# Kernel tuning notes

Measured on AMD Instinct MI355X. Metric: run time of the kernel, lower is better.

Reference implementation:

```python
import jax, jax.numpy as jnp
import numpy as np
import itertools

D_MODEL = 1024
TEMP = 0.3


def _hypercube(n):
    # all 2^n corners of {-1,+1}^n, matching generate_hypercube(n)
    return jnp.asarray(np.array(list(itertools.product([-1.0, 1.0], repeat=n)), dtype=np.float32))


def setup_inputs() -> dict:
    key = jax.random.key(0)
    ks = jax.random.split(key, 12)
    B, T, D = 8, 4096, D_MODEL
    s = 0.02
    return {
        "x": jax.random.normal(ks[0], (B, T, D), dtype=jnp.float32),
        "codes_l1": _hypercube(3),   # (8, 3)
        "codes_l2": _hypercube(6),   # (64, 6)
        "w_to_l1": jax.random.normal(ks[1], (D, 3), dtype=jnp.float32) * s,
        "w_from_l1": jax.random.normal(ks[2], (3, D), dtype=jnp.float32) * s,
        "w_to_l2": jax.random.normal(ks[3], (D, 6), dtype=jnp.float32) * s,
        "w_from_l2": jax.random.normal(ks[4], (6, D), dtype=jnp.float32) * s,
        "w_to_l3u": jax.random.normal(ks[5], (D, 6), dtype=jnp.float32) * s,
        "w_to_l3l": jax.random.normal(ks[6], (D, 6), dtype=jnp.float32) * s,
        "w_from_l3": jax.random.normal(ks[7], (12, D), dtype=jnp.float32) * s,
        "w_gate": jax.random.normal(ks[8], (D, 3), dtype=jnp.float32) * s,
        "b_gate": jnp.zeros((3,), dtype=jnp.float32),
        "temp_l1": jnp.log(jnp.float32(TEMP)),
        "temp_l2": jnp.log(jnp.float32(TEMP * 0.7)),
        "temp_l3": jnp.log(jnp.float32(TEMP * 0.5)),
        "scale_l1": jnp.float32(0.1),
        "scale_l2": jnp.float32(0.05),
        "scale_l3": jnp.float32(0.02),
    }


def _soft_quantize(z, codes, temp_log):
    # z: (B, T, n); codes: (K, n) -> (B, T, n)
    temp = jnp.clip(jnp.exp(temp_log), 0.01, 5.0)
    # Euclidean cdist: (B, T, K)
    dists = jnp.sqrt(jnp.sum(jnp.square(z[..., None, :] - codes), axis=-1))
    weights = jax.nn.softmax(-dists / temp, axis=-1)
    return weights @ codes


def reference(x, codes_l1, codes_l2, w_to_l1, w_from_l1, w_to_l2, w_from_l2,
              w_to_l3u, w_to_l3l, w_from_l3, w_gate, b_gate,
              temp_l1, temp_l2, temp_l3, scale_l1, scale_l2, scale_l3):
    # gate uses detached x
    gate = jax.nn.softmax(jax.lax.stop_gradient(x) @ w_gate + b_gate, axis=-1)  # (B,T,3)

    # Level 1: Z2^3
    q1 = _soft_quantize(x @ w_to_l1, codes_l1, temp_l1)
    out_l1 = q1 @ w_from_l1

    # Level 2: Z2^6
    q2 = _soft_quantize(x @ w_to_l2, codes_l2, temp_l2)
    out_l2 = q2 @ w_from_l2

    # Level 3: Z2^12 = two Z2^6 halves
    q3u = _soft_quantize(x @ w_to_l3u, codes_l2, temp_l3)
    q3l = _soft_quantize(x @ w_to_l3l, codes_l2, temp_l3)
    out_l3 = jnp.concatenate([q3u, q3l], axis=-1) @ w_from_l3

    out = (gate[..., 0:1] * scale_l1 * out_l1
           + gate[..., 1:2] * scale_l2 * out_l2
           + gate[..., 2:3] * scale_l3 * out_l3)
    gate_means = jnp.mean(gate, axis=(0, 1))  # stats dict analogue: (3,)
    return x + out, gate_means
```

## Files before the change

### kernel.cpp

```cpp
#include <hip/hip_runtime.h>
#include <stdint.h>


#define DM 1024
#define TPB 64
#define OUT_OFF ((size_t)33554432)
#define NTOK 32768
#define NSLOT 32
#define WSA_OFF 32768

typedef float f32x4 __attribute__((ext_vector_type(4)));
typedef short bf16x8 __attribute__((ext_vector_type(8)));

typedef const __attribute__((address_space(1))) unsigned int* gas1_t;
typedef __attribute__((address_space(3))) unsigned int* las3_t;

__device__ __forceinline__ void gl_lds16(const void* g, void* l){
  __builtin_amdgcn_global_load_lds((gas1_t)g, (las3_t)l, 16, 0, 0);
}

__device__ __forceinline__ short f2bf(float f){
  unsigned u = __builtin_bit_cast(unsigned, f);
  unsigned r = u + 0x7fffu + ((u >> 16) & 1u);
  return (short)(r >> 16);
}

template<int NB>
__device__ __forceinline__ void softq(const float* z, float invt, float* q){
  constexpr int K = 1 << NB;
  float d[K];
  float dmin = 3.4e38f;
#pragma unroll
  for (int j = 0; j < K; ++j){
    float acc = 0.f;
#pragma unroll
    for (int i = 0; i < NB; ++i){
      float c = ((j >> (NB-1-i)) & 1) ? 1.f : -1.f;
      float t = z[i] - c;
      acc = fmaf(t, t, acc);
    }
    float dj = sqrtf(acc);
    d[j] = dj;
    dmin = fminf(dmin, dj);
  }
  float S = 0.f;
  float s1[NB];
#pragma unroll
  for (int i = 0; i < NB; ++i) s1[i] = 0.f;
#pragma unroll
  for (int j = 0; j < K; ++j){
    float wj = __expf((dmin - d[j]) * invt);
    S += wj;
#pragma unroll
    for (int i = 0; i < NB; ++i)
      if ((j >> (NB-1-i)) & 1) s1[i] += wj;
  }
  float rS = 1.f / S;
#pragma unroll
  for (int i = 0; i < NB; ++i) q[i] = 2.f * s1[i] * rS - 1.f;
}

__global__ __launch_bounds__(256) void pack_kernel(
    const float* __restrict__ w_to_l1,  const float* __restrict__ w_to_l2,
    const float* __restrict__ w_to_l3u, const float* __restrict__ w_to_l3l,
    const float* __restrict__ w_gate,
    const float* __restrict__ w_from_l1, const float* __restrict__ w_from_l2,
    const float* __restrict__ w_from_l3,
    short* __restrict__ wsF, float* __restrict__ wsA)
{
  int base = blockIdx.x*4096 + threadIdx.x*16;
#pragma unroll
  for (int q = 0; q < 16; ++q){
    int e = base + q;
    float v;
    if (e < 32768){
      int s  = e >> 10;
      int nf = (e >> 9) & 1;
      int ll = (e >> 3) & 63;
      int j  = e & 7;
      int k  = s*32 + ((ll >> 4) << 3) + j;
      int n  = nf*16 + (ll & 15);
      if      (n < 3)  v = w_gate  [k*3 + n];
      else if (n < 6)  v = w_to_l1 [k*3 + (n-3)];
      else if (n < 12) v = w_to_l2 [k*6 + (n-6)];
      else if (n < 18) v = w_to_l3u[k*6 + (n-12)];
      else if (n < 24) v = w_to_l3l[k*6 + (n-18)];
      else             v = 0.f;
    } else {
      int e2  = e - 32768;
      int f   = e2 / 384;
      int rem = e2 - f*384;
      int ll  = rem >> 3;
      int j   = e2 & 7;
      int k   = ((ll >> 4) << 3) + j;
      int dd  = f*16 + (ll & 15);
      if      (k < 3)  v = w_from_l1[k*DM + dd];
      else if (k < 9)  v = w_from_l2[(k-3)*DM + dd];
      else if (k < 21) v = w_from_l3[(k-9)*DM + dd];
      else             v = 0.f;
    }
    wsF[e] = f2bf(v);
  }
  if (blockIdx.x == 0){
    wsA[threadIdx.x]       = 0.f;
    wsA[threadIdx.x + 256] = 0.f;
  }
}

__global__ __launch_bounds__(256, 2) void hq8_kernel(
    const float* __restrict__ x, const short* __restrict__ wsF,
    const float* __restrict__ b_gate,
    const float* __restrict__ t1p, const float* __restrict__ t2p, const float* __restrict__ t3p,
    const float* __restrict__ s1p, const float* __restrict__ s2p, const float* __restrict__ s3p,
    float* __restrict__ wsA, float* __restrict__ out)
{
  __shared__ alignas(16) char smem[65536];

  const int tid  = threadIdx.x;
  const int l    = tid & 63;
  const int wv   = tid >> 6;
  const int kg   = l >> 4;
  const int ln16 = l & 15;
  const int tokBase = blockIdx.x * TPB + wv*16;

  char*  W  = smem + wv*16384;
  float* Cw = reinterpret_cast<float*>(W + 8192);
  float* Pw = reinterpret_cast<float*>(W + 12544);
  short* Vw = reinterpret_cast<short*>(W + 14720);

  const float invt1 = 1.f / fminf(fmaxf(__expf(t1p[0]), 0.01f), 5.0f);
  const float invt2 = 1.f / fminf(fmaxf(__expf(t2p[0]), 0.01f), 5.0f);
  const float invt3 = 1.f / fminf(fmaxf(__expf(t3p[0]), 0.01f), 5.0f);
  const float s1v = s1p[0], s2v = s2p[0], s3v = s3p[0];
  const float bg0 = b_gate[0], bg1 = b_gate[1], bg2 = b_gate[2];

  {
    f32x4 acc0 = {0.f,0.f,0.f,0.f}, acc1 = {0.f,0.f,0.f,0.f};
    const int lr0 = l >> 5;
    const int cbp = l & 31;
#pragma unroll
    for (int i = 0; i < 8; ++i){
      int lr = i*2 + lr0;
      gl_lds16(x + (size_t)(tokBase + lr)*DM + (cbp ^ (lr & 7))*4,
               W + i*1024 + l*16);
    }
#pragma unroll
    for (int t = 0; t < 8; ++t){
      const int buf = t & 1;
      bf16x8 bfr[8];
#pragma unroll
      for (int s2 = 0; s2 < 8; ++s2)
        bfr[s2] = *reinterpret_cast<const bf16x8*>(&wsF[(t*8 + s2)*512 + l*8]);
      __builtin_amdgcn_sched_barrier(0);
      if (t < 7){
#pragma unroll
        for (int i = 0; i < 8; ++i){
          int lr = i*2 + lr0;
          gl_lds16(x + (size_t)(tokBase + lr)*DM + (t+1)*128 + (cbp ^ (lr & 7))*4,
                   W + (buf^1)*8192 + i*1024 + l*16);
        }
        asm volatile("s_waitcnt vmcnt(8)" ::: "memory");
      } else {
        asm volatile("s_waitcnt vmcnt(0)" ::: "memory");
      }
      const char* abase = W + buf*8192 + ln16*512;
#pragma unroll
      for (int s = 0; s < 4; ++s){
        float4 xa = *reinterpret_cast<const float4*>(abase + ((s*8 + kg*2 + 0) ^ (ln16 & 7))*16);
        float4 xb = *reinterpret_cast<const float4*>(abase + ((s*8 + kg*2 + 1) ^ (ln16 & 7))*16);
        bf16x8 af;
        af[0]=f2bf(xa.x); af[1]=f2bf(xa.y); af[2]=f2bf(xa.z); af[3]=f2bf(xa.w);
        af[4]=f2bf(xb.x); af[5]=f2bf(xb.y); af[6]=f2bf(xb.z); af[7]=f2bf(xb.w);
        acc0 = __builtin_amdgcn_mfma_f32_16x16x32_bf16(af, bfr[s*2+0], acc0, 0, 0, 0);
        acc1 = __builtin_amdgcn_mfma_f32_16x16x32_bf16(af, bfr[s*2+1], acc1, 0, 0, 0);
      }
    }
#pragma unroll
    for (int r = 0; r < 4; ++r){
      int row = kg*4 + r;
      Pw[row*34 + ln16]      = acc0[r];
      Pw[row*34 + 16 + ln16] = acc1[r];
    }
  }

  const short* wsFC = wsF + 32768;
  bf16x8 bwc0={0,0,0,0,0,0,0,0}, bwc1=bwc0, bwc2=bwc0, bwc3=bwc0;
  {
#pragma unroll
    for (int j = 0; j < 4; ++j){
      int lr = j*4 + (l >> 4);
      gl_lds16(x + (size_t)(tokBase + lr)*DM + ((l & 15) ^ (lr & 7))*4,
               W + j*1024 + l*16);
    }
    if (kg < 3){
      bwc0 = *reinterpret_cast<const bf16x8*>(&wsFC[0*384 + l*8]);
      bwc1 = *reinterpret_cast<const bf16x8*>(&wsFC[1*384 + l*8]);
      bwc2 = *reinterpret_cast<const bf16x8*>(&wsFC[2*384 + l*8]);
      bwc3 = *reinterpret_cast<const bf16x8*>(&wsFC[3*384 + l*8]);
    }
#pragma unroll
    for (int j = 0; j < 4; ++j){
      int lr = j*4 + (l >> 4);
      gl_lds16(x + (size_t)(tokBase + lr)*DM + 64 + ((l & 15) ^ (lr & 7))*4,
               W + 4096 + j*1024 + l*16);
    }
  }

  float qv[6] = {0,0,0,0,0,0};
  float myscale = 0.f, g1s2v = 0.f, g2s3v = 0.f;
  float sg0 = 0.f, sg1 = 0.f, sg2 = 0.f;
  {
    const int t  = ln16;
    const int gi = kg;
    const int base = (gi == 3) ? 0 : 6 + gi*6;
    float z[6];
#pragma unroll
    for (int i = 0; i < 6; ++i) z[i] = Pw[t*34 + base + i];
    if (gi == 3){
      float g0l = z[0] + bg0;
      float g1l = z[1] + bg1;
      float g2l = z[2] + bg2;
      float m  = fmaxf(g0l, fmaxf(g1l, g2l));
      float e0 = __expf(g0l - m), e1 = __expf(g1l - m), e2 = __expf(g2l - m);
      float rs = 1.f / (e0 + e1 + e2);
      float g0 = e0*rs, g1 = e1*rs, g2 = e2*rs;
      myscale = g0 * s1v;
      g1s2v   = g1 * s2v;
      g2s3v   = g2 * s3v;
      float z1[3] = {z[3], z[4], z[5]};
      softq<3>(z1, invt1, qv);
      sg0 = g0; sg1 = g1; sg2 = g2;
#pragma unroll
      for (int mm = 1; mm < 16; mm <<= 1){
        sg0 += __shfl_xor(sg0, mm, 64);
        sg1 += __shfl_xor(sg1, mm, 64);
        sg2 += __shfl_xor(sg2, mm, 64);
      }
    } else {
      float invt = (gi == 0) ? invt2 : invt3;
      softq<6>(z, invt, qv);
    }
    float gs1 = __shfl(g1s2v, 48 + t, 64);
    float gs2 = __shfl(g2s3v, 48 + t, 64);
    if (gi == 3){
#pragma unroll
      for (int i = 0; i < 3; ++i) Vw[t*40 + i] = f2bf(myscale * qv[i]);
      Vw[t*40 + 21] = 0; Vw[t*40 + 22] = 0; Vw[t*40 + 23] = 0;
    } else {
      float sc = (gi == 0) ? gs1 : gs2;
      int voff = 3 + gi*6;
#pragma unroll
      for (int i = 0; i < 6; ++i) Vw[t*40 + voff + i] = f2bf(sc * qv[i]);
    }
  }

  bf16x8 aV = {0,0,0,0,0,0,0,0};
  if (kg < 3)
    aV = *reinterpret_cast<const bf16x8*>(&Vw[ln16*40 + kg*8]);
  const f32x4 z4 = {0.f,0.f,0.f,0.f};
  const int rl = l >> 2;
  const int cs = l & 3;

#pragma unroll
  for (int c = 0; c < 16; ++c){
    if (c == 0 || c == 15) asm volatile("s_waitcnt vmcnt(4)" ::: "memory");
    else                   asm volatile("s_waitcnt vmcnt(8)" ::: "memory");
    __builtin_amdgcn_sched_barrier(0);
    {
      f32x4 d0 = __builtin_amdgcn_mfma_f32_16x16x32_bf16(aV, bwc0, z4, 0, 0, 0);
      f32x4 d1 = __builtin_amdgcn_mfma_f32_16x16x32_bf16(aV, bwc1, z4, 0, 0, 0);
      f32x4 d2 = __builtin_amdgcn_mfma_f32_16x16x32_bf16(aV, bwc2, z4, 0, 0, 0);
      f32x4 d3 = __builtin_amdgcn_mfma_f32_16x16x32_bf16(aV, bwc3, z4, 0, 0, 0);
#pragma unroll
      for (int r = 0; r < 4; ++r){
        int rowb = (kg*4 + r)*68;
        Cw[rowb +  0 + ln16] = d0[r];
        Cw[rowb + 16 + ln16] = d1[r];
        Cw[rowb + 32 + ln16] = d2[r];
        Cw[rowb + 48 + ln16] = d3[r];
      }
    }
    __builtin_amdgcn_sched_barrier(0);
    bf16x8 bwn0 = bwc0, bwn1 = bwc1, bwn2 = bwc2, bwn3 = bwc3;
    if (c < 15 && kg < 3){
      bwn0 = *reinterpret_cast<const bf16x8*>(&wsFC[((c+1)*4+0)*384 + l*8]);
      bwn1 = *reinterpret_cast<const bf16x8*>(&wsFC[((c+1)*4+1)*384 + l*8]);
      bwn2 = *reinterpret_cast<const bf16x8*>(&wsFC[((c+1)*4+2)*384 + l*8]);
      bwn3 = *reinterpret_cast<const bf16x8*>(&wsFC[((c+1)*4+3)*384 + l*8]);
    }
    __builtin_amdgcn_sched_barrier(0);
    asm volatile("s_waitcnt lgkmcnt(0)" ::: "memory");
    __builtin_amdgcn_sched_barrier(0);
#pragma unroll
    for (int q = 0; q < 4; ++q){
      int bi = cs + 4*q;
      f32x4 xv = *reinterpret_cast<const f32x4*>(
          W + (c & 1)*4096 + rl*256 + ((bi ^ (rl & 7)))*16);
      f32x4 cv = *reinterpret_cast<const f32x4*>(&Cw[rl*68 + bi*4]);
      f32x4 ov = xv + cv;
      *reinterpret_cast<f32x4*>(&out[(size_t)(tokBase + rl)*DM + c*64 + bi*4]) = ov;
    }
    __builtin_amdgcn_sched_barrier(0);
    if (c < 14){
#pragma unroll
      for (int j = 0; j < 4; ++j){
        int lr = j*4 + (l >> 4);
        gl_lds16(x + (size_t)(tokBase + lr)*DM + (c+2)*64 + ((l & 15) ^ (lr & 7))*4,
                 W + (c & 1)*4096 + j*1024 + l*16);
      }
    }
    bwc0 = bwn0; bwc1 = bwn1; bwc2 = bwn2; bwc3 = bwn3;
  }

  if (l == 48){
    float* slot = wsA + ((blockIdx.x*4 + wv) & (NSLOT-1))*16;
    atomicAdd(slot + 0, sg0);
    atomicAdd(slot + 1, sg1);
    atomicAdd(slot + 2, sg2);
  }
}

__global__ void finalize_kernel(const float* __restrict__ wsA, float* __restrict__ out){
  if (threadIdx.x < 3){
    float s = 0.f;
    for (int j = 0; j < NSLOT; ++j) s += wsA[j*16 + threadIdx.x];
    out[OUT_OFF + threadIdx.x] = s * (1.f / (float)NTOK);
  }
}

extern "C" void kernel_launch(void* const* d_in, const int* in_sizes, int n_in,
                              void* d_out, int out_size, void* d_ws, size_t ws_size,
                              hipStream_t stream){
  (void)in_sizes; (void)n_in; (void)ws_size; (void)out_size;
  const float* x         = (const float*)d_in[0];
  const float* w_to_l1   = (const float*)d_in[3];
  const float* w_from_l1 = (const float*)d_in[4];
  const float* w_to_l2   = (const float*)d_in[5];
  const float* w_from_l2 = (const float*)d_in[6];
  const float* w_to_l3u  = (const float*)d_in[7];
  const float* w_to_l3l  = (const float*)d_in[8];
  const float* w_from_l3 = (const float*)d_in[9];
  const float* w_gate    = (const float*)d_in[10];
  const float* b_gate    = (const float*)d_in[11];
  const float* t1 = (const float*)d_in[12];
  const float* t2 = (const float*)d_in[13];
  const float* t3 = (const float*)d_in[14];
  const float* s1 = (const float*)d_in[15];
  const float* s2 = (const float*)d_in[16];
  const float* s3 = (const float*)d_in[17];
  float* out  = (float*)d_out;
  short* wsF  = (short*)d_ws;
  float* wsA  = (float*)d_ws + WSA_OFF;

  pack_kernel<<<dim3(14), dim3(256), 0, stream>>>(
      w_to_l1, w_to_l2, w_to_l3u, w_to_l3l, w_gate,
      w_from_l1, w_from_l2, w_from_l3, wsF, wsA);
  hq8_kernel<<<dim3(512), dim3(256), 0, stream>>>(
      x, wsF, b_gate, t1, t2, t3, s1, s2, s3, wsA, out);
  finalize_kernel<<<dim3(1), dim3(64), 0, stream>>>(wsA, out);
}
```

Measured before the change: 81.03 us.

## Split fused kernel into down-projection and up-projection kernels via workspace

Splits the single fused kernel into two. The first kernel computes the projections, gate and soft-quantization and writes the per-token scaled code vectors to a workspace. The second kernel reads those vectors back, does the up-projection MFMA and adds x to produce the output. This simplifies each kernel's pipeline and register use, but it reads x a second time from memory (128MB extra traffic) and drops the hand-tuned double-buffered residual prefetch.

```diff
diff --git a/kernel.cpp b/kernel.cpp
--- a/kernel.cpp
+++ b/kernel.cpp
@@ -3,11 +3,11 @@
 
 
 #define DM 1024
-#define TPB 64
 #define OUT_OFF ((size_t)33554432)
 #define NTOK 32768
 #define NSLOT 32
-#define WSA_OFF 32768
+#define WSV_OFF 65536
+#define WSA_OFFF 557056
 
 typedef float f32x4 __attribute__((ext_vector_type(4)));
 typedef short bf16x8 __attribute__((ext_vector_type(8)));
@@ -107,12 +107,63 @@
   }
 }
 
-__global__ __launch_bounds__(256, 2) void hq8_kernel(
+__device__ __forceinline__ void quant16(const float* Pw, short* Vw, int l,
+    float invt1, float invt2, float invt3, float s1v, float s2v, float s3v,
+    float bg0, float bg1, float bg2, float& sg0, float& sg1, float& sg2)
+{
+  const int t  = l & 15;
+  const int gi = l >> 4;
+  const int base = (gi == 3) ? 0 : 6 + gi*6;
+  float z[6];
+#pragma unroll
+  for (int i = 0; i < 6; ++i) z[i] = Pw[t*34 + base + i];
+  float qv[6] = {0,0,0,0,0,0};
+  float myscale = 0.f, g1s2v = 0.f, g2s3v = 0.f;
+  if (gi == 3){
+    float g0l = z[0] + bg0;
+    float g1l = z[1] + bg1;
+    float g2l = z[2] + bg2;
+    float m  = fmaxf(g0l, fmaxf(g1l, g2l));
+    float e0 = __expf(g0l - m), e1 = __expf(g1l - m), e2 = __expf(g2l - m);
+    float rs = 1.f / (e0 + e1 + e2);
+    float g0 = e0*rs, g1 = e1*rs, g2 = e2*rs;
+    myscale = g0 * s1v;
+    g1s2v   = g1 * s2v;
+    g2s3v   = g2 * s3v;
+    float z1[3] = {z[3], z[4], z[5]};
+    softq<3>(z1, invt1, qv);
+    float a0 = g0, a1 = g1, a2 = g2;
+#pragma unroll
+    for (int mm = 1; mm < 16; mm <<= 1){
+      a0 += __shfl_xor(a0, mm, 64);
+      a1 += __shfl_xor(a1, mm, 64);
+      a2 += __shfl_xor(a2, mm, 64);
+    }
+    sg0 += a0; sg1 += a1; sg2 += a2;
+  } else {
+    float invt = (gi == 0) ? invt2 : invt3;
+    softq<6>(z, invt, qv);
+  }
+  float gs1 = __shfl(g1s2v, 48 + t, 64);
+  float gs2 = __shfl(g2s3v, 48 + t, 64);
+  if (gi == 3){
+#pragma unroll
+    for (int i = 0; i < 3; ++i) Vw[t*40 + i] = f2bf(myscale * qv[i]);
+    Vw[t*40 + 21] = 0; Vw[t*40 + 22] = 0; Vw[t*40 + 23] = 0;
+  } else {
+    float sc = (gi == 0) ? gs1 : gs2;
+    int voff = 3 + gi*6;
+#pragma unroll
+    for (int i = 0; i < 6; ++i) Vw[t*40 + voff + i] = f2bf(sc * qv[i]);
+  }
+}
+
+__global__ __launch_bounds__(256, 2) void down_kernel(
     const float* __restrict__ x, const short* __restrict__ wsF,
     const float* __restrict__ b_gate,
     const float* __restrict__ t1p, const float* __restrict__ t2p, const float* __restrict__ t3p,
     const float* __restrict__ s1p, const float* __restrict__ s2p, const float* __restrict__ s3p,
-    float* __restrict__ wsA, float* __restrict__ out)
+    float* __restrict__ wsA, short* __restrict__ wsV)
 {
   __shared__ alignas(16) char smem[65536];
 
@@ -121,10 +172,9 @@
   const int wv   = tid >> 6;
   const int kg   = l >> 4;
   const int ln16 = l & 15;
-  const int tokBase = blockIdx.x * TPB + wv*16;
+  const size_t tokBase = (size_t)blockIdx.x*64 + wv*16;
 
   char*  W  = smem + wv*16384;
-  float* Cw = reinterpret_cast<float*>(W + 8192);
   float* Pw = reinterpret_cast<float*>(W + 12544);
   short* Vw = reinterpret_cast<short*>(W + 14720);
 
@@ -133,6 +183,7 @@
   const float invt3 = 1.f / fminf(fmaxf(__expf(t3p[0]), 0.01f), 5.0f);
   const float s1v = s1p[0], s2v = s2p[0], s3v = s3p[0];
   const float bg0 = b_gate[0], bg1 = b_gate[1], bg2 = b_gate[2];
+  float sg0 = 0.f, sg1 = 0.f, sg2 = 0.f;
 
   {
     f32x4 acc0 = {0.f,0.f,0.f,0.f}, acc1 = {0.f,0.f,0.f,0.f};
@@ -141,8 +192,7 @@
 #pragma unroll
     for (int i = 0; i < 8; ++i){
       int lr = i*2 + lr0;
-      gl_lds16(x + (size_t)(tokBase + lr)*DM + (cbp ^ (lr & 7))*4,
-               W + i*1024 + l*16);
+      gl_lds16(x + (tokBase + lr)*DM + (cbp ^ (lr & 7))*4, W + i*1024 + l*16);
     }
 #pragma unroll
     for (int t = 0; t < 8; ++t){
@@ -156,13 +206,14 @@
 #pragma unroll
         for (int i = 0; i < 8; ++i){
           int lr = i*2 + lr0;
-          gl_lds16(x + (size_t)(tokBase + lr)*DM + (t+1)*128 + (cbp ^ (lr & 7))*4,
+          gl_lds16(x + (tokBase + lr)*DM + (t+1)*128 + (cbp ^ (lr & 7))*4,
                    W + (buf^1)*8192 + i*1024 + l*16);
         }
         asm volatile("s_waitcnt vmcnt(8)" ::: "memory");
       } else {
         asm volatile("s_waitcnt vmcnt(0)" ::: "memory");
       }
+      __builtin_amdgcn_sched_barrier(0);
       const char* abase = W + buf*8192 + ln16*512;
 #pragma unroll
       for (int s = 0; s < 4; ++s){
@@ -183,133 +234,12 @@
     }
   }
 
-  const short* wsFC = wsF + 32768;
-  bf16x8 bwc0={0,0,0,0,0,0,0,0}, bwc1=bwc0, bwc2=bwc0, bwc3=bwc0;
+  quant16(Pw, Vw, l, invt1, invt2, invt3, s1v, s2v, s3v, bg0, bg1, bg2, sg0, sg1, sg2);
   {
-#pragma unroll
-    for (int j = 0; j < 4; ++j){
-      int lr = j*4 + (l >> 4);
-      gl_lds16(x + (size_t)(tokBase + lr)*DM + ((l & 15) ^ (lr & 7))*4,
-               W + j*1024 + l*16);
-    }
-    if (kg < 3){
-      bwc0 = *reinterpret_cast<const bf16x8*>(&wsFC[0*384 + l*8]);
-      bwc1 = *reinterpret_cast<const bf16x8*>(&wsFC[1*384 + l*8]);
-      bwc2 = *reinterpret_cast<const bf16x8*>(&wsFC[2*384 + l*8]);
-      bwc3 = *reinterpret_cast<const bf16x8*>(&wsFC[3*384 + l*8]);
-    }
-#pragma unroll
-    for (int j = 0; j < 4; ++j){
-      int lr = j*4 + (l >> 4);
-      gl_lds16(x + (size_t)(tokBase + lr)*DM + 64 + ((l & 15) ^ (lr & 7))*4,
-               W + 4096 + j*1024 + l*16);
-    }
-  }
-
-  float qv[6] = {0,0,0,0,0,0};
-  float myscale = 0.f, g1s2v = 0.f, g2s3v = 0.f;
-  float sg0 = 0.f, sg1 = 0.f, sg2 = 0.f;
-  {
-    const int t  = ln16;
-    const int gi = kg;
-    const int base = (gi == 3) ? 0 : 6 + gi*6;
-    float z[6];
-#pragma unroll
-    for (int i = 0; i < 6; ++i) z[i] = Pw[t*34 + base + i];
-    if (gi == 3){
-      float g0l = z[0] + bg0;
-      float g1l = z[1] + bg1;
-      float g2l = z[2] + bg2;
-      float m  = fmaxf(g0l, fmaxf(g1l, g2l));
-      float e0 = __expf(g0l - m), e1 = __expf(g1l - m), e2 = __expf(g2l - m);
-      float rs = 1.f / (e0 + e1 + e2);
-      float g0 = e0*rs, g1 = e1*rs, g2 = e2*rs;
-      myscale = g0 * s1v;
-      g1s2v   = g1 * s2v;
-      g2s3v   = g2 * s3v;
-      float z1[3] = {z[3], z[4], z[5]};
-      softq<3>(z1, invt1, qv);
-      sg0 = g0; sg1 = g1; sg2 = g2;
-#pragma unroll
-      for (int mm = 1; mm < 16; mm <<= 1){
-        sg0 += __shfl_xor(sg0, mm, 64);
-        sg1 += __shfl_xor(sg1, mm, 64);
-        sg2 += __shfl_xor(sg2, mm, 64);
-      }
-    } else {
-      float invt = (gi == 0) ? invt2 : invt3;
-      softq<6>(z, invt, qv);
-    }
-    float gs1 = __shfl(g1s2v, 48 + t, 64);
-    float gs2 = __shfl(g2s3v, 48 + t, 64);
-    if (gi == 3){
-#pragma unroll
-      for (int i = 0; i < 3; ++i) Vw[t*40 + i] = f2bf(myscale * qv[i]);
-      Vw[t*40 + 21] = 0; Vw[t*40 + 22] = 0; Vw[t*40 + 23] = 0;
-    } else {
-      float sc = (gi == 0) ? gs1 : gs2;
-      int voff = 3 + gi*6;
-#pragma unroll
-      for (int i = 0; i < 6; ++i) Vw[t*40 + voff + i] = f2bf(sc * qv[i]);
-    }
-  }
-
-  bf16x8 aV = {0,0,0,0,0,0,0,0};
-  if (kg < 3)
-    aV = *reinterpret_cast<const bf16x8*>(&Vw[ln16*40 + kg*8]);
-  const f32x4 z4 = {0.f,0.f,0.f,0.f};
-  const int rl = l >> 2;
-  const int cs = l & 3;
-
-#pragma unroll
-  for (int c = 0; c < 16; ++c){
-    if (c == 0 || c == 15) asm volatile("s_waitcnt vmcnt(4)" ::: "memory");
-    else                   asm volatile("s_waitcnt vmcnt(8)" ::: "memory");
-    __builtin_amdgcn_sched_barrier(0);
-    {
-      f32x4 d0 = __builtin_amdgcn_mfma_f32_16x16x32_bf16(aV, bwc0, z4, 0, 0, 0);
-      f32x4 d1 = __builtin_amdgcn_mfma_f32_16x16x32_bf16(aV, bwc1, z4, 0, 0, 0);
-      f32x4 d2 = __builtin_amdgcn_mfma_f32_16x16x32_bf16(aV, bwc2, z4, 0, 0, 0);
-      f32x4 d3 = __builtin_amdgcn_mfma_f32_16x16x32_bf16(aV, bwc3, z4, 0, 0, 0);
-#pragma unroll
-      for (int r = 0; r < 4; ++r){
-        int rowb = (kg*4 + r)*68;
-        Cw[rowb +  0 + ln16] = d0[r];
-        Cw[rowb + 16 + ln16] = d1[r];
-        Cw[rowb + 32 + ln16] = d2[r];
-        Cw[rowb + 48 + ln16] = d3[r];
-      }
-    }
-    __builtin_amdgcn_sched_barrier(0);
-    bf16x8 bwn0 = bwc0, bwn1 = bwc1, bwn2 = bwc2, bwn3 = bwc3;
-    if (c < 15 && kg < 3){
-      bwn0 = *reinterpret_cast<const bf16x8*>(&wsFC[((c+1)*4+0)*384 + l*8]);
-      bwn1 = *reinterpret_cast<const bf16x8*>(&wsFC[((c+1)*4+1)*384 + l*8]);
-      bwn2 = *reinterpret_cast<const bf16x8*>(&wsFC[((c+1)*4+2)*384 + l*8]);
-      bwn3 = *reinterpret_cast<const bf16x8*>(&wsFC[((c+1)*4+3)*384 + l*8]);
-    }
-    __builtin_amdgcn_sched_barrier(0);
-    asm volatile("s_waitcnt lgkmcnt(0)" ::: "memory");
-    __builtin_amdgcn_sched_barrier(0);
-#pragma unroll
-    for (int q = 0; q < 4; ++q){
-      int bi = cs + 4*q;
-      f32x4 xv = *reinterpret_cast<const f32x4*>(
-          W + (c & 1)*4096 + rl*256 + ((bi ^ (rl & 7)))*16);
-      f32x4 cv = *reinterpret_cast<const f32x4*>(&Cw[rl*68 + bi*4]);
-      f32x4 ov = xv + cv;
-      *reinterpret_cast<f32x4*>(&out[(size_t)(tokBase + rl)*DM + c*64 + bi*4]) = ov;
-    }
-    __builtin_amdgcn_sched_barrier(0);
-    if (c < 14){
-#pragma unroll
-      for (int j = 0; j < 4; ++j){
-        int lr = j*4 + (l >> 4);
-        gl_lds16(x + (size_t)(tokBase + lr)*DM + (c+2)*64 + ((l & 15) ^ (lr & 7))*4,
-                 W + (c & 1)*4096 + j*1024 + l*16);
-      }
-    }
-    bwc0 = bwn0; bwc1 = bwn1; bwc2 = bwn2; bwc3 = bwn3;
+    int row = l >> 2, seg = l & 3;
+    bf16x8 v = {0,0,0,0,0,0,0,0};
+    if (seg < 3) v = *reinterpret_cast<const bf16x8*>(&Vw[row*40 + seg*8]);
+    *reinterpret_cast<bf16x8*>(&wsV[(tokBase + row)*32 + seg*8]) = v;
   }
 
   if (l == 48){
@@ -317,6 +247,60 @@
     atomicAdd(slot + 0, sg0);
     atomicAdd(slot + 1, sg1);
     atomicAdd(slot + 2, sg2);
+  }
+}
+
+__global__ __launch_bounds__(256) void up_kernel(
+    const short* __restrict__ wsF, const short* __restrict__ wsV,
+    const float* __restrict__ x, float* __restrict__ out)
+{
+  __shared__ float C[64*68];
+
+  const int tid  = threadIdx.x;
+  const int l    = tid & 63;
+  const int wv   = tid >> 6;
+  const int kg   = l >> 4;
+  const int ln16 = l & 15;
+  const int tb   = blockIdx.x * 64;
+  const short* wsFC = wsF + 32768;
+
+  bf16x8 aV = {0,0,0,0,0,0,0,0};
+  if (kg < 3)
+    aV = *reinterpret_cast<const bf16x8*>(&wsV[(size_t)(tb + wv*16 + ln16)*32 + kg*8]);
+
+  const f32x4 z4 = {0.f,0.f,0.f,0.f};
+  const int rrow = tid >> 4;
+  const int rcol = (tid & 15) * 4;
+
+#pragma unroll 1
+  for (int c = 0; c < 16; ++c){
+    float4 xv[4];
+#pragma unroll
+    for (int p = 0; p < 4; ++p){
+      int row = p*16 + rrow;
+      xv[p] = *reinterpret_cast<const float4*>(&x[(size_t)(tb + row)*DM + c*64 + rcol]);
+    }
+#pragma unroll
+    for (int ff = 0; ff < 4; ++ff){
+      bf16x8 bfr = {0,0,0,0,0,0,0,0};
+      if (kg < 3)
+        bfr = *reinterpret_cast<const bf16x8*>(&wsFC[(c*4+ff)*384 + l*8]);
+      f32x4 dd = __builtin_amdgcn_mfma_f32_16x16x32_bf16(aV, bfr, z4, 0, 0, 0);
+#pragma unroll
+      for (int r = 0; r < 4; ++r)
+        C[(wv*16 + kg*4 + r)*68 + ff*16 + ln16] = dd[r];
+    }
+    __syncthreads();
+#pragma unroll
+    for (int p = 0; p < 4; ++p){
+      int row = p*16 + rrow;
+      float4 cv = *reinterpret_cast<const float4*>(&C[row*68 + rcol]);
+      float4 ov;
+      ov.x = xv[p].x + cv.x; ov.y = xv[p].y + cv.y;
+      ov.z = xv[p].z + cv.z; ov.w = xv[p].w + cv.w;
+      *reinterpret_cast<float4*>(&out[(size_t)(tb + row)*DM + c*64 + rcol]) = ov;
+    }
+    __syncthreads();
   }
 }
 
@@ -350,12 +334,15 @@
   const float* s3 = (const float*)d_in[17];
   float* out  = (float*)d_out;
   short* wsF  = (short*)d_ws;
-  float* wsA  = (float*)d_ws + WSA_OFF;
+  short* wsV  = (short*)d_ws + WSV_OFF;
+  float* wsA  = (float*)d_ws + WSA_OFFF;
 
   pack_kernel<<<dim3(14), dim3(256), 0, stream>>>(
       w_to_l1, w_to_l2, w_to_l3u, w_to_l3l, w_gate,
       w_from_l1, w_from_l2, w_from_l3, wsF, wsA);
-  hq8_kernel<<<dim3(512), dim3(256), 0, stream>>>(
-      x, wsF, b_gate, t1, t2, t3, s1, s2, s3, wsA, out);
+  down_kernel<<<dim3(512), dim3(256), 0, stream>>>(
+      x, wsF, b_gate, t1, t2, t3, s1, s2, s3, wsA, wsV);
+  up_kernel<<<dim3(512), dim3(256), 0, stream>>>(
+      wsF, wsV, x, out);
   finalize_kernel<<<dim3(1), dim3(64), 0, stream>>>(wsA, out);
 }
```

Result: slower. 96.37 us (+18.9%).
